# Kernel optimization log

Hardware: AMD Instinct MI355X
Metric: run time of the kernel (lower is better)

## Reference

```python
import jax, jax.numpy as jnp
import numpy as np

B, C, H, W = 64, 64, 56, 56
MID = 2 * C  # two output nodes concatenated
EPS = 1e-5


def _conv1x1(x, w):
    # x: [B,C,H,W], w: [O,C] (1x1 conv kernel squeezed)
    return jnp.einsum('bchw,oc->bohw', x, w)


def _bn(x, g, b, m, v):
    # eval-mode BatchNorm2d with running stats
    sc = g * jax.lax.rsqrt(v + EPS)
    return x * sc[None, :, None, None] + (b - m * sc)[None, :, None, None]


def _maxpool3(x):
    # MaxPool2d(kernel=3, stride=1, padding=1)
    return jax.lax.reduce_window(x, -jnp.inf, jax.lax.max,
                                 (1, 1, 3, 3), (1, 1, 1, 1),
                                 [(0, 0), (0, 0), (1, 1), (1, 1)])


def _avgpool3(x):
    # AvgPool2d(kernel=3, stride=1, padding=1), count_include_pad=True -> /9
    s = jax.lax.reduce_window(x, 0.0, jax.lax.add,
                              (1, 1, 3, 3), (1, 1, 1, 1),
                              [(0, 0), (0, 0), (1, 1), (1, 1)])
    return s * (1.0 / 9.0)


def setup_inputs() -> dict:
    key = jax.random.key(0)
    ks = jax.random.split(key, 11)
    x = jax.random.normal(ks[0], (B, C, H, W), dtype=jnp.float32)
    w1 = jax.random.normal(ks[1], (C, C), dtype=jnp.float32) * 0.1
    w2 = jax.random.normal(ks[2], (C, MID), dtype=jnp.float32) * 0.1
    bn1_g = 1.0 + 0.1 * jax.random.normal(ks[3], (C,), dtype=jnp.float32)
    bn1_b = 0.1 * jax.random.normal(ks[4], (C,), dtype=jnp.float32)
    bn1_m = 0.1 * jax.random.normal(ks[5], (C,), dtype=jnp.float32)
    bn1_v = jax.random.uniform(ks[6], (C,), minval=0.5, maxval=1.5, dtype=jnp.float32)
    bn2_g = 1.0 + 0.1 * jax.random.normal(ks[7], (C,), dtype=jnp.float32)
    bn2_b = 0.1 * jax.random.normal(ks[8], (C,), dtype=jnp.float32)
    bn2_m = 0.1 * jax.random.normal(ks[9], (C,), dtype=jnp.float32)
    bn2_v = jax.random.uniform(ks[10], (C,), minval=0.5, maxval=1.5, dtype=jnp.float32)
    return dict(x=x, w1=w1, w2=w2,
                bn1_g=bn1_g, bn1_b=bn1_b, bn1_m=bn1_m, bn1_v=bn1_v,
                bn2_g=bn2_g, bn2_b=bn2_b, bn2_m=bn2_m, bn2_v=bn2_v)


def reference(x, w1, w2, bn1_g, bn1_b, bn1_m, bn1_v, bn2_g, bn2_b, bn2_m, bn2_v):
    # DAG g = [[[0,1],[1,2]], [[4,3],[3]], [[5,3],[3,100]], [[4,3],[100]]]
    # topoSort order: [0, 2, 1, 3]; output nodes (ordered): [2, 3]
    node0 = jax.nn.relu(_bn(_conv1x1(x, w1), bn1_g, bn1_b, bn1_m, bn1_v))
    node1 = _maxpool3(node0)            # op type 4, pred {0}
    node2 = _avgpool3(node0)            # op type 5, pred {0}
    node3 = _maxpool3(node1) + _maxpool3(node2)  # op type 4, preds {1,2}, summed
    cat = jnp.concatenate([node2, node3], axis=1)  # [B, 2C, H, W]
    out = jax.nn.relu(_bn(_conv1x1(cat, w2), bn2_g, bn2_b, bn2_m, bn2_v))
    return out
```

## Files before the change

### kernel.cpp

```cpp
#include <hip/hip_runtime.h>
#include <cstddef>

#define EPS 1e-5f
static constexpr int Bn = 64, Cn = 64, Hn = 56, Wn = 56, HWn = Hn * Wn;
static constexpr int CSTR = 136;

typedef __attribute__((ext_vector_type(8))) short short8;
typedef __attribute__((ext_vector_type(8))) unsigned short ushort8;
typedef __attribute__((ext_vector_type(4))) float floatx4;
typedef __attribute__((ext_vector_type(16))) float floatx16;
typedef __attribute__((ext_vector_type(4))) unsigned int uintx4;
typedef __attribute__((ext_vector_type(2))) unsigned int uintx2;

__device__ __forceinline__ unsigned pack_rne(float a, float b) {
    unsigned ua = __float_as_uint(a), ub = __float_as_uint(b);
    ua = ua + 0x7fffu + ((ua >> 16) & 1u);
    ub = ub + 0x7fffu + ((ub >> 16) & 1u);
    return __builtin_amdgcn_perm(ub, ua, 0x07060302);
}
__device__ __forceinline__ unsigned pack_trunc(float a, float b) {
    return __builtin_amdgcn_perm(__float_as_uint(b), __float_as_uint(a), 0x07060302);
}
__device__ __forceinline__ ushort8 pmax(ushort8 a, ushort8 b) {
    return __builtin_elementwise_max(a, b);
}
__device__ __forceinline__ float bf_lo(unsigned u) { return __uint_as_float(u << 16); }
__device__ __forceinline__ float bf_hi(unsigned u) { return __uint_as_float(u & 0xffff0000u); }


__global__ __launch_bounds__(256) void k1_conv1(
    const float* __restrict__ x, const float* __restrict__ w1,
    const float* __restrict__ bg, const float* __restrict__ bb,
    const float* __restrict__ bm, const float* __restrict__ bv,
    unsigned short* __restrict__ node0)
{
    __shared__ float scs[64], shs[64];
    const int tid = threadIdx.x;
    if (tid < 64) {
        float sc = bg[tid] * rsqrtf(bv[tid] + EPS);
        scs[tid] = sc;
        shs[tid] = bb[tid] - bm[tid] * sc;
    }
    __syncthreads();
    const int lane = tid & 63;
    const int wv   = tid >> 6;
    const int m    = lane & 15;
    const int quad = lane >> 4;

    short8 afr[4][2];
    float shv[16];
    #pragma unroll
    for (int t = 0; t < 4; ++t) {
        const float sc = scs[t * 16 + m];
        #pragma unroll
        for (int kk = 0; kk < 2; ++kk) {
            const float* wp = w1 + (t * 16 + m) * 64 + kk * 32 + quad * 8;
            floatx4 f0 = *(const floatx4*)wp;
            floatx4 f1 = *(const floatx4*)(wp + 4);
            uintx4 u;
            u.x = pack_rne(f0[0] * sc, f0[1] * sc);
            u.y = pack_rne(f0[2] * sc, f0[3] * sc);
            u.z = pack_rne(f1[0] * sc, f1[1] * sc);
            u.w = pack_rne(f1[2] * sc, f1[3] * sc);
            afr[t][kk] = *(short8*)&u;
        }
        #pragma unroll
        for (int i = 0; i < 4; ++i) shv[t * 4 + i] = shs[t * 16 + quad * 4 + i];
    }

    #pragma unroll 1
    for (int tt = 0; tt < 4; ++tt) {
        const long P0 = (long)blockIdx.x * 256 + tt * 64;
        const int b = (int)(P0 / HWn);
        const int p0 = (int)(P0 - (long)b * HWn);
        const int p = p0 + wv * 16 + m;

        floatx4 acc[4];
        #pragma unroll
        for (int t = 0; t < 4; ++t) acc[t] = (floatx4){0.f, 0.f, 0.f, 0.f};

        #pragma unroll
        for (int kk = 0; kk < 2; ++kk) {
            float xv[8];
            #pragma unroll
            for (int j = 0; j < 8; ++j)
                xv[j] = x[(size_t)(b * 64 + kk * 32 + quad * 8 + j) * HWn + p];
            uintx4 u;
            u.x = pack_trunc(xv[0], xv[1]);
            u.y = pack_trunc(xv[2], xv[3]);
            u.z = pack_trunc(xv[4], xv[5]);
            u.w = pack_trunc(xv[6], xv[7]);
            short8 bfr = *(short8*)&u;
            #pragma unroll
            for (int t = 0; t < 4; ++t)
                acc[t] = __builtin_amdgcn_mfma_f32_16x16x32_bf16(afr[t][kk], bfr, acc[t], 0, 0, 0);
        }

        const int chunkbase = (quad >> 1);
        const int j0 = (quad & 1) * 4;
        #pragma unroll
        for (int t = 0; t < 4; ++t) {
            float v0 = acc[t][0] + shv[t * 4 + 0]; v0 = v0 > 0.f ? v0 : 0.f;
            float v1 = acc[t][1] + shv[t * 4 + 1]; v1 = v1 > 0.f ? v1 : 0.f;
            float v2 = acc[t][2] + shv[t * 4 + 2]; v2 = v2 > 0.f ? v2 : 0.f;
            float v3 = acc[t][3] + shv[t * 4 + 3]; v3 = v3 > 0.f ? v3 : 0.f;
            uintx2 st;
            st.x = pack_rne(v0, v1);
            st.y = pack_rne(v2, v3);
            int chunk = t * 2 + chunkbase;
            *(uintx2*)(node0 + ((size_t)(b * 8 + chunk) * HWn + p0 + wv * 16 + m) * 8 + j0) = st;
        }
    }
}

__global__ __launch_bounds__(512, 4) void k23_fused(
    const unsigned short* __restrict__ node0, const float* __restrict__ w2,
    const float* __restrict__ bg, const float* __restrict__ bb,
    const float* __restrict__ bm, const float* __restrict__ bv,
    float* __restrict__ out)
{
    __shared__ unsigned short ct[224 * CSTR];
    __shared__ unsigned short wl[1024 * 8];
    __shared__ float scs[64], shs[64];
    const int tid = threadIdx.x;
    if (tid < 64) {
        float sc = bg[tid] * rsqrtf(bv[tid] + EPS);
        scs[tid] = sc;
        shs[tid] = bb[tid] - bm[tid] * sc;
    }
    #pragma unroll
    for (int q = 0; q < 2; ++q) {
        int ci = tid * 2 + q;
        int lane_ = ci & 63, tk = ci >> 6;
        int t = tk >> 3, kt = tk & 7, n_ = lane_ & 31, h_ = lane_ >> 5;
        const float* wp = w2 + (t * 32 + n_) * 128 + kt * 16 + h_ * 8;
        floatx4 f0 = *(const floatx4*)wp;
        floatx4 f1 = *(const floatx4*)(wp + 4);
        uintx4 u;
        u.x = pack_rne(f0[0], f0[1]);
        u.y = pack_rne(f0[2], f0[3]);
        u.z = pack_rne(f1[0], f1[1]);
        u.w = pack_rne(f1[2], f1[3]);
        *(uintx4*)(wl + (size_t)ci * 8) = u;
    }

    const int lane = tid & 63;
    const int wv = tid >> 6;
    const int b = blockIdx.x / 14;
    const int band = blockIdx.x % 14;
    const int lo = band * 4;
    const int col = lane;
    const bool act = col < Wn;
    const unsigned short* base = node0 + ((size_t)(b * 8 + wv) * HWn) * 8;

    {
        const ushort8 zz = (ushort8)0;
        float hs1[8], hs2[8];
        ushort8 h5a = zz, h5b = zz, h5c = zz, h5d = zz, nh1 = zz, nh2 = zz;
        #pragma unroll
        for (int j = 0; j < 8; ++j) hs1[j] = hs2[j] = 0.f;

        #pragma unroll
        for (int r = lo - 2; r <= lo + 5; ++r) {
            ushort8 d[5];
            #pragma unroll
            for (int dd = 0; dd < 5; ++dd) {
                int cc = col + dd - 2;
                bool ok = act && ((unsigned)cc < (unsigned)Wn) && ((unsigned)r < (unsigned)Hn);
                d[dd] = ok ? *(const ushort8*)(base + (size_t)(r * Wn + cc) * 8) : zz;
            }
            ushort8 hm5 = pmax(pmax(pmax(d[0], d[1]), pmax(d[2], d[3])), d[4]);
            ushort8 m5 = pmax(pmax(pmax(h5a, h5b), pmax(h5c, h5d)), hm5);
            h5a = h5b; h5b = h5c; h5c = h5d; h5d = hm5;

            const uintx4 ul = *(const uintx4*)&d[1];
            const uintx4 uv = *(const uintx4*)&d[2];
            const uintx4 ur = *(const uintx4*)&d[3];
            float a2[8];
            const int r2 = r - 1, r3 = r - 2;
            const bool v2 = (unsigned)r2 < (unsigned)Hn;
            #pragma unroll
            for (int w = 0; w < 4; ++w) {
                float hsum0 = bf_lo(ul[w]) + bf_lo(uv[w]) + bf_lo(ur[w]);
                float hsum1 = bf_hi(ul[w]) + bf_hi(uv[w]) + bf_hi(ur[w]);
                a2[w * 2 + 0] = v2 ? (hs2[w * 2 + 0] + hs1[w * 2 + 0] + hsum0) * (1.f / 9.f) : 0.f;
                a2[w * 2 + 1] = v2 ? (hs2[w * 2 + 1] + hs1[w * 2 + 1] + hsum1) * (1.f / 9.f) : 0.f;
                hs2[w * 2 + 0] = hs1[w * 2 + 0]; hs1[w * 2 + 0] = hsum0;
                hs2[w * 2 + 1] = hs1[w * 2 + 1]; hs1[w * 2 + 1] = hsum1;
            }
            uintx4 ap;
            ap.x = pack_rne(a2[0], a2[1]);
            ap.y = pack_rne(a2[2], a2[3]);
            ap.z = pack_rne(a2[4], a2[5]);
            ap.w = pack_rne(a2[6], a2[7]);
            uintx4 al, ar;
            #pragma unroll
            for (int w = 0; w < 4; ++w) {
                unsigned u = ap[w];
                unsigned lu = __shfl_up(u, 1);
                unsigned ru = __shfl_down(u, 1);
                al[w] = (lane == 0) ? 0u : lu;
                ar[w] = (lane == 63) ? 0u : ru;
            }
            ushort8 nh = pmax(pmax(*(ushort8*)&al, *(ushort8*)&ap), *(ushort8*)&ar);
            ushort8 m3 = pmax(pmax(nh2, nh1), nh);
            nh2 = nh1; nh1 = nh;

            if (act && r2 >= lo && r2 < lo + 4) {
                int px = (r2 - lo) * Wn + col;
                *(uintx4*)(ct + (size_t)px * CSTR + wv * 8) = ap;
            }
            if (act && r3 >= lo && r3 < lo + 4) {
                const uintx4 u5 = *(const uintx4*)&m5;
                const uintx4 u3 = *(const uintx4*)&m3;
                uintx4 st;
                #pragma unroll
                for (int w = 0; w < 4; ++w)
                    st[w] = pack_rne(bf_lo(u5[w]) + bf_lo(u3[w]), bf_hi(u5[w]) + bf_hi(u3[w]));
                int px = (r3 - lo) * Wn + col;
                *(uintx4*)(ct + (size_t)px * CSTR + 64 + wv * 8) = st;
            }
        }
    }
    __syncthreads();

    if (wv >= 7) return;
    const int n = lane & 31;
    const int h = lane >> 5;

    short8 afr[2][8];
    #pragma unroll
    for (int t = 0; t < 2; ++t)
        #pragma unroll
        for (int kt = 0; kt < 8; ++kt)
            afr[t][kt] = *(const short8*)(wl + ((size_t)((t * 8 + kt) * 64 + lane)) * 8);

    const int px0 = wv * 32;
    floatx16 acc0, acc1;
    #pragma unroll
    for (int i = 0; i < 16; ++i) { acc0[i] = 0.f; acc1[i] = 0.f; }

    #pragma unroll
    for (int kt = 0; kt < 8; ++kt) {
        short8 bfr = *(const short8*)(ct + (size_t)(px0 + n) * CSTR + kt * 16 + h * 8);
        acc0 = __builtin_amdgcn_mfma_f32_32x32x16_bf16(afr[0][kt], bfr, acc0, 0, 0, 0);
        acc1 = __builtin_amdgcn_mfma_f32_32x32x16_bf16(afr[1][kt], bfr, acc1, 0, 0, 0);
    }

    float* ob = out + (size_t)b * 64 * HWn + lo * Wn + px0 + n;
    #pragma unroll
    for (int r = 0; r < 16; ++r) {
        int o = (r & 3) + 8 * (r >> 2) + 4 * h;
        float v0 = fmaf(acc0[r], scs[o], shs[o]);
        ob[(size_t)o * HWn] = v0 > 0.f ? v0 : 0.f;
        float v1 = fmaf(acc1[r], scs[o + 32], shs[o + 32]);
        ob[(size_t)(o + 32) * HWn] = v1 > 0.f ? v1 : 0.f;
    }
}

extern "C" void kernel_launch(void* const* d_in, const int* in_sizes, int n_in,
                              void* d_out, int out_size, void* d_ws, size_t ws_size,
                              hipStream_t stream)
{
    const float* x   = (const float*)d_in[0];
    const float* w1  = (const float*)d_in[1];
    const float* w2  = (const float*)d_in[2];
    const float* b1g = (const float*)d_in[3];
    const float* b1b = (const float*)d_in[4];
    const float* b1m = (const float*)d_in[5];
    const float* b1v = (const float*)d_in[6];
    const float* b2g = (const float*)d_in[7];
    const float* b2b = (const float*)d_in[8];
    const float* b2m = (const float*)d_in[9];
    const float* b2v = (const float*)d_in[10];

    float* out = (float*)d_out;
    unsigned short* node0 = (unsigned short*)d_ws;

    k1_conv1<<<dim3(784), dim3(256), 0, stream>>>(x, w1, b1g, b1b, b1m, b1v, node0);
    k23_fused<<<dim3(Bn * 14), dim3(512), 0, stream>>>(node0, w2, b2g, b2b, b2m, b2v, out);
}
```

Measured before the change: 170.6 us.

## Prefetch conv1 inputs, double fused band height, swizzle LDS, stage coalesced output

The first kernel now issues the next tile's x loads before the current tile's MFMAs, so global loads overlap compute. The fused kernel processes 8-row bands in two 4-row passes, which cuts the halo rows recomputed per block and halves the grid. It also replaces the padded LDS stride with an XOR swizzle to avoid bank conflicts. Outputs are staged through LDS so they are written as coalesced float4 stores. The cost is more barriers, higher register pressure and fewer blocks to fill the GPU.

```diff
diff --git a/kernel.cpp b/kernel.cpp
--- a/kernel.cpp
+++ b/kernel.cpp
@@ -3,7 +3,6 @@
 
 #define EPS 1e-5f
 static constexpr int Bn = 64, Cn = 64, Hn = 56, Wn = 56, HWn = Hn * Wn;
-static constexpr int CSTR = 136;
 
 typedef __attribute__((ext_vector_type(8))) short short8;
 typedef __attribute__((ext_vector_type(8))) unsigned short ushort8;
@@ -46,6 +45,7 @@
     const int wv   = tid >> 6;
     const int m    = lane & 15;
     const int quad = lane >> 4;
+    const int qoff = quad * 8;
 
     short8 afr[4][2];
     float shv[16];
@@ -54,7 +54,7 @@
         const float sc = scs[t * 16 + m];
         #pragma unroll
         for (int kk = 0; kk < 2; ++kk) {
-            const float* wp = w1 + (t * 16 + m) * 64 + kk * 32 + quad * 8;
+            const float* wp = w1 + (t * 16 + m) * 64 + kk * 32 + qoff;
             floatx4 f0 = *(const floatx4*)wp;
             floatx4 f1 = *(const floatx4*)(wp + 4);
             uintx4 u;
@@ -68,12 +68,31 @@
         for (int i = 0; i < 4; ++i) shv[t * 4 + i] = shs[t * 16 + quad * 4 + i];
     }
 
-    #pragma unroll 1
+    float xv[2][16];
+    {
+        const int P = blockIdx.x * 256;
+        const int b = P / HWn, p0 = P - b * HWn;
+        const float* xb = x + (size_t)b * 64 * HWn + p0 + wv * 16 + m;
+        #pragma unroll
+        for (int j = 0; j < 8; ++j) {
+            xv[0][j]     = xb[(size_t)(qoff + j) * HWn];
+            xv[0][8 + j] = xb[(size_t)(32 + qoff + j) * HWn];
+        }
+    }
+
+    #pragma unroll
     for (int tt = 0; tt < 4; ++tt) {
-        const long P0 = (long)blockIdx.x * 256 + tt * 64;
-        const int b = (int)(P0 / HWn);
-        const int p0 = (int)(P0 - (long)b * HWn);
-        const int p = p0 + wv * 16 + m;
+        const int cur = tt & 1, nxt = cur ^ 1;
+        if (tt < 3) {
+            const int P = blockIdx.x * 256 + (tt + 1) * 64;
+            const int b = P / HWn, p0 = P - b * HWn;
+            const float* xb = x + (size_t)b * 64 * HWn + p0 + wv * 16 + m;
+            #pragma unroll
+            for (int j = 0; j < 8; ++j) {
+                xv[nxt][j]     = xb[(size_t)(qoff + j) * HWn];
+                xv[nxt][8 + j] = xb[(size_t)(32 + qoff + j) * HWn];
+            }
+        }
 
         floatx4 acc[4];
         #pragma unroll
@@ -81,21 +100,19 @@
 
         #pragma unroll
         for (int kk = 0; kk < 2; ++kk) {
-            float xv[8];
-            #pragma unroll
-            for (int j = 0; j < 8; ++j)
-                xv[j] = x[(size_t)(b * 64 + kk * 32 + quad * 8 + j) * HWn + p];
             uintx4 u;
-            u.x = pack_trunc(xv[0], xv[1]);
-            u.y = pack_trunc(xv[2], xv[3]);
-            u.z = pack_trunc(xv[4], xv[5]);
-            u.w = pack_trunc(xv[6], xv[7]);
+            u.x = pack_trunc(xv[cur][kk * 8 + 0], xv[cur][kk * 8 + 1]);
+            u.y = pack_trunc(xv[cur][kk * 8 + 2], xv[cur][kk * 8 + 3]);
+            u.z = pack_trunc(xv[cur][kk * 8 + 4], xv[cur][kk * 8 + 5]);
+            u.w = pack_trunc(xv[cur][kk * 8 + 6], xv[cur][kk * 8 + 7]);
             short8 bfr = *(short8*)&u;
             #pragma unroll
             for (int t = 0; t < 4; ++t)
                 acc[t] = __builtin_amdgcn_mfma_f32_16x16x32_bf16(afr[t][kk], bfr, acc[t], 0, 0, 0);
         }
 
+        const int P = blockIdx.x * 256 + tt * 64;
+        const int b = P / HWn, p0 = P - b * HWn;
         const int chunkbase = (quad >> 1);
         const int j0 = (quad & 1) * 4;
         #pragma unroll
@@ -119,7 +136,7 @@
     const float* __restrict__ bm, const float* __restrict__ bv,
     float* __restrict__ out)
 {
-    __shared__ unsigned short ct[224 * CSTR];
+    __shared__ unsigned short ct[224 * 128];
     __shared__ unsigned short wl[1024 * 8];
     __shared__ float scs[64], shs[64];
     const int tid = threadIdx.x;
@@ -143,25 +160,31 @@
         u.w = pack_rne(f1[2], f1[3]);
         *(uintx4*)(wl + (size_t)ci * 8) = u;
     }
+    __syncthreads();
 
     const int lane = tid & 63;
     const int wv = tid >> 6;
-    const int b = blockIdx.x / 14;
-    const int band = blockIdx.x % 14;
-    const int lo = band * 4;
+    const int b = blockIdx.x / 7;
+    const int lo = (blockIdx.x % 7) * 8;
     const int col = lane;
     const bool act = col < Wn;
     const unsigned short* base = node0 + ((size_t)(b * 8 + wv) * HWn) * 8;
 
-    {
-        const ushort8 zz = (ushort8)0;
-        float hs1[8], hs2[8];
-        ushort8 h5a = zz, h5b = zz, h5c = zz, h5d = zz, nh1 = zz, nh2 = zz;
-        #pragma unroll
-        for (int j = 0; j < 8; ++j) hs1[j] = hs2[j] = 0.f;
-
-        #pragma unroll
-        for (int r = lo - 2; r <= lo + 5; ++r) {
+    const ushort8 zz = (ushort8)0;
+    float hs1[8], hs2[8];
+    ushort8 h5a = zz, h5b = zz, h5c = zz, h5d = zz, nh1 = zz, nh2 = zz;
+    uintx4 apq; apq.x = 0u; apq.y = 0u; apq.z = 0u; apq.w = 0u;
+    #pragma unroll
+    for (int j = 0; j < 8; ++j) hs1[j] = hs2[j] = 0.f;
+
+    #pragma unroll 1
+    for (int q = 0; q < 2; ++q) {
+        const int rstart = lo - 2 + (q ? 8 : 0);
+        const int niter = q ? 4 : 8;
+        #pragma unroll
+        for (int i = 0; i < 8; ++i) {
+            if (i >= niter) break;
+            const int r = rstart + i;
             ushort8 d[5];
             #pragma unroll
             for (int dd = 0; dd < 5; ++dd) {
@@ -177,14 +200,13 @@
             const uintx4 uv = *(const uintx4*)&d[2];
             const uintx4 ur = *(const uintx4*)&d[3];
             float a2[8];
-            const int r2 = r - 1, r3 = r - 2;
-            const bool v2 = (unsigned)r2 < (unsigned)Hn;
+            const bool vr = (unsigned)(r - 1) < (unsigned)Hn;
             #pragma unroll
             for (int w = 0; w < 4; ++w) {
                 float hsum0 = bf_lo(ul[w]) + bf_lo(uv[w]) + bf_lo(ur[w]);
                 float hsum1 = bf_hi(ul[w]) + bf_hi(uv[w]) + bf_hi(ur[w]);
-                a2[w * 2 + 0] = v2 ? (hs2[w * 2 + 0] + hs1[w * 2 + 0] + hsum0) * (1.f / 9.f) : 0.f;
-                a2[w * 2 + 1] = v2 ? (hs2[w * 2 + 1] + hs1[w * 2 + 1] + hsum1) * (1.f / 9.f) : 0.f;
+                a2[w * 2 + 0] = vr ? (hs2[w * 2 + 0] + hs1[w * 2 + 0] + hsum0) * (1.f / 9.f) : 0.f;
+                a2[w * 2 + 1] = vr ? (hs2[w * 2 + 1] + hs1[w * 2 + 1] + hsum1) * (1.f / 9.f) : 0.f;
                 hs2[w * 2 + 0] = hs1[w * 2 + 0]; hs1[w * 2 + 0] = hsum0;
                 hs2[w * 2 + 1] = hs1[w * 2 + 1]; hs1[w * 2 + 1] = hsum1;
             }
@@ -206,55 +228,71 @@
             ushort8 m3 = pmax(pmax(nh2, nh1), nh);
             nh2 = nh1; nh1 = nh;
 
-            if (act && r2 >= lo && r2 < lo + 4) {
-                int px = (r2 - lo) * Wn + col;
-                *(uintx4*)(ct + (size_t)px * CSTR + wv * 8) = ap;
-            }
-            if (act && r3 >= lo && r3 < lo + 4) {
+            const int ro = r - 2;
+            if (act && ro >= lo && ro < lo + 8) {
+                const int pxt = ((ro - lo) & 3) * Wn + col;
+                const int sw = pxt & 15;
+                *(uintx4*)(ct + (size_t)pxt * 128 + (size_t)(wv ^ sw) * 8) = apq;
                 const uintx4 u5 = *(const uintx4*)&m5;
                 const uintx4 u3 = *(const uintx4*)&m3;
                 uintx4 st;
                 #pragma unroll
                 for (int w = 0; w < 4; ++w)
                     st[w] = pack_rne(bf_lo(u5[w]) + bf_lo(u3[w]), bf_hi(u5[w]) + bf_hi(u3[w]));
-                int px = (r3 - lo) * Wn + col;
-                *(uintx4*)(ct + (size_t)px * CSTR + 64 + wv * 8) = st;
-            }
-        }
-    }
-    __syncthreads();
-
-    if (wv >= 7) return;
-    const int n = lane & 31;
-    const int h = lane >> 5;
-
-    short8 afr[2][8];
-    #pragma unroll
-    for (int t = 0; t < 2; ++t)
-        #pragma unroll
-        for (int kt = 0; kt < 8; ++kt)
-            afr[t][kt] = *(const short8*)(wl + ((size_t)((t * 8 + kt) * 64 + lane)) * 8);
-
-    const int px0 = wv * 32;
-    floatx16 acc0, acc1;
-    #pragma unroll
-    for (int i = 0; i < 16; ++i) { acc0[i] = 0.f; acc1[i] = 0.f; }
-
-    #pragma unroll
-    for (int kt = 0; kt < 8; ++kt) {
-        short8 bfr = *(const short8*)(ct + (size_t)(px0 + n) * CSTR + kt * 16 + h * 8);
-        acc0 = __builtin_amdgcn_mfma_f32_32x32x16_bf16(afr[0][kt], bfr, acc0, 0, 0, 0);
-        acc1 = __builtin_amdgcn_mfma_f32_32x32x16_bf16(afr[1][kt], bfr, acc1, 0, 0, 0);
-    }
-
-    float* ob = out + (size_t)b * 64 * HWn + lo * Wn + px0 + n;
-    #pragma unroll
-    for (int r = 0; r < 16; ++r) {
-        int o = (r & 3) + 8 * (r >> 2) + 4 * h;
-        float v0 = fmaf(acc0[r], scs[o], shs[o]);
-        ob[(size_t)o * HWn] = v0 > 0.f ? v0 : 0.f;
-        float v1 = fmaf(acc1[r], scs[o + 32], shs[o + 32]);
-        ob[(size_t)(o + 32) * HWn] = v1 > 0.f ? v1 : 0.f;
+                *(uintx4*)(ct + (size_t)pxt * 128 + (size_t)((8 + wv) ^ sw) * 8) = st;
+            }
+            apq = ap;
+        }
+        __syncthreads();
+
+        floatx16 acc0, acc1;
+        const int n = lane & 31;
+        const int h = lane >> 5;
+        if (wv < 7) {
+            short8 afr[2][8];
+            #pragma unroll
+            for (int t = 0; t < 2; ++t)
+                #pragma unroll
+                for (int kt = 0; kt < 8; ++kt)
+                    afr[t][kt] = *(const short8*)(wl + ((size_t)((t * 8 + kt) * 64 + lane)) * 8);
+            const int px = wv * 32 + n;
+            #pragma unroll
+            for (int i = 0; i < 16; ++i) { acc0[i] = 0.f; acc1[i] = 0.f; }
+            #pragma unroll
+            for (int kt = 0; kt < 8; ++kt) {
+                const int u = (kt * 2 + h) ^ (px & 15);
+                short8 bfr = *(const short8*)(ct + (size_t)px * 128 + (size_t)u * 8);
+                acc0 = __builtin_amdgcn_mfma_f32_32x32x16_bf16(afr[0][kt], bfr, acc0, 0, 0, 0);
+                acc1 = __builtin_amdgcn_mfma_f32_32x32x16_bf16(afr[1][kt], bfr, acc1, 0, 0, 0);
+            }
+        }
+        __syncthreads();
+        if (wv < 7) {
+            float* ot = (float*)ct;
+            const int px = wv * 32 + n;
+            #pragma unroll
+            for (int r = 0; r < 16; ++r) {
+                int o = (r & 3) + 8 * (r >> 2) + 4 * h;
+                float v0 = fmaf(acc0[r], scs[o], shs[o]);
+                ot[o * 224 + px] = v0 > 0.f ? v0 : 0.f;
+                float v1 = fmaf(acc1[r], scs[o + 32], shs[o + 32]);
+                ot[(o + 32) * 224 + px] = v1 > 0.f ? v1 : 0.f;
+            }
+        }
+        __syncthreads();
+        {
+            const float* ot = (const float*)ct;
+            const size_t obase = (size_t)b * 64 * HWn + (size_t)(lo + 4 * q) * Wn;
+            #pragma unroll
+            for (int it = 0; it < 7; ++it) {
+                int ci = it * 512 + tid;
+                int o = ci / 56;
+                int c4 = (ci - o * 56) * 4;
+                floatx4 v = *(const floatx4*)(ot + ci * 4);
+                *(floatx4*)(out + obase + (size_t)o * HWn + c4) = v;
+            }
+        }
+        __syncthreads();
     }
 }
 
@@ -278,5 +316,5 @@
     unsigned short* node0 = (unsigned short*)d_ws;
 
     k1_conv1<<<dim3(784), dim3(256), 0, stream>>>(x, w1, b1g, b1b, b1m, b1v, node0);
-    k23_fused<<<dim3(Bn * 14), dim3(512), 0, stream>>>(node0, w2, b2g, b2b, b2m, b2v, out);
-}
+    k23_fused<<<dim3(Bn * 7), dim3(512), 0, stream>>>(node0, w2, b2g, b2b, b2m, b2v, out);
+}
```

After: 185.9 us. +8.9%, slower.
